# Performance work log

Hardware: AMD Instinct MI355X
Metric: run time of the kernel (lower is better)

Reference implementation:

```python
import jax, jax.numpy as jnp
import numpy as np

N, K, D_IN, D_H, D_A, N_CLS = 8192, 10, 1024, 512, 256, 4


def setup_inputs() -> dict:
    key = jax.random.key(0)
    ks = jax.random.split(key, 20)
    def lin(k, fan_in, shape):
        return jax.random.normal(k, shape, dtype=jnp.float32) / np.sqrt(fan_in)
    return {
        "x_path": jax.random.normal(ks[0], (N, D_IN), dtype=jnp.float32),
        "cluster_id": jax.random.randint(ks[1], (N,), 0, K),
        # per-cluster phi MLP (Linear 1024->512, ReLU, Linear 512->512, ReLU); dropout = eval identity
        "W1": lin(ks[2], D_IN, (K, D_IN, D_H)), "b1": jnp.zeros((K, D_H), jnp.float32),
        "W2": lin(ks[3], D_H, (K, D_H, D_H)), "b2": jnp.zeros((K, D_H), jnp.float32),
        # attention_net fc: Linear 512->512 + ReLU
        "fc_W": lin(ks[4], D_H, (D_H, D_H)), "fc_b": jnp.zeros((D_H,), jnp.float32),
        # Attn_Net_Gated: a=tanh(Va), b=sigmoid(Vb), A=(a*b)@Vc
        "Va": lin(ks[5], D_H, (D_H, D_A)), "ba": jnp.zeros((D_A,), jnp.float32),
        "Vb": lin(ks[6], D_H, (D_H, D_A)), "bb": jnp.zeros((D_A,), jnp.float32),
        "Vc": lin(ks[7], D_A, (D_A, 1)), "bc": jnp.zeros((1,), jnp.float32),
        # rho: Linear 512->256 + ReLU
        "rho_W": lin(ks[8], D_H, (D_H, D_A)), "rho_b": jnp.zeros((D_A,), jnp.float32),
        # classifier: Linear 256->4
        "cls_W": lin(ks[9], D_A, (D_A, N_CLS)), "cls_b": jnp.zeros((N_CLS,), jnp.float32),
    }


def reference(x_path, cluster_id, W1, b1, W2, b2, fc_W, fc_b,
              Va, ba, Vb, bb, Vc, bc, rho_W, rho_b, cls_W, cls_b):
    # mask[k, n] = 1 if patch n belongs to cluster k
    mask = (cluster_id[None, :] == jnp.arange(K)[:, None]).astype(x_path.dtype)  # [K, N]

    # per-cluster 2-layer MLP applied to all patches, masked mean-pool (= AdaptiveAvgPool1d(1))
    def phi(W1i, b1i, W2i, b2i):
        h = jax.nn.relu(x_path @ W1i + b1i)          # [N, 512]
        return jax.nn.relu(h @ W2i + b2i)            # [N, 512]
    y = jax.vmap(phi)(W1, b1, W2, b2)                # [K, N, 512]
    cnt = mask.sum(axis=1)                           # [K]
    pooled = jnp.einsum('kn,knd->kd', mask, y) / jnp.maximum(cnt, 1.0)[:, None]  # [K, 512]
    # empty cluster -> zeros (matches torch.zeros((1,512)) branch since b terms are zero via where)
    pooled = jnp.where(cnt[:, None] > 0, pooled, 0.0)

    # attention_net: fc + gated attention
    h = jax.nn.relu(pooled @ fc_W + fc_b)            # [K, 512]
    a = jnp.tanh(h @ Va + ba)                        # [K, 256]
    b = jax.nn.sigmoid(h @ Vb + bb)                  # [K, 256]
    A = (a * b) @ Vc + bc                            # [K, 1]
    A = jax.nn.softmax(A.T, axis=1)                  # [1, K]
    h_path = A @ h                                   # [1, 512]
    h_path = jax.nn.relu(h_path @ rho_W + rho_b)[0]  # [256]
    logits = (h_path @ cls_W + cls_b)[None, :]       # [1, 4]
    Y_hat = jnp.argmax(logits, axis=1, keepdims=True)
    hazards = jax.nn.sigmoid(logits)
    S = jnp.cumprod(1.0 - hazards, axis=1)
    return hazards, S, Y_hat
```

## Files before the change

kernel.cpp:

```cpp
#include <hip/hip_runtime.h>
#include <math.h>

#define NPATCH 8192
#define KC     10
#define DIN    1024
#define DH     512
#define DA     256
#define NCLS   4

#define TM  32

typedef unsigned short u16;
typedef short bf16x8 __attribute__((ext_vector_type(8)));
typedef float f32x4  __attribute__((ext_vector_type(4)));

#define OFF_CNT   0
#define OFF_BAR   48
#define OFF_IDX   64
#define OFF_PSUM  327744
#define OFF_H     348224
#define OFF_H2    368768
#define OFF_SRED  369792
#define OFF_W1P   373888
#define OFF_W2P   10859648

__device__ __forceinline__ u16 f2bf(float f) {
  union { float f; unsigned u; } v; v.f = f;
  unsigned r = (v.u + 0x7fffu + ((v.u >> 16) & 1u)) >> 16;
  return (u16)r;
}

__device__ __forceinline__ unsigned cvtpk(float lo, float hi) {
  unsigned r;
  asm("v_cvt_pk_bf16_f32 %0, %1, %2" : "=v"(r) : "v"(lo), "v"(hi));
  return r;
}

struct __align__(8) U16x4 { u16 x, y, z, w; };
union BF8U { bf16x8 v; unsigned u[4]; };

__device__ __forceinline__ void dma16(const u16* gp, u16* lp) {
  __builtin_amdgcn_global_load_lds(
      (const __attribute__((address_space(1))) void*)gp,
      (__attribute__((address_space(3))) void*)lp, 16, 0, 0);
}

#define W1_TILES (KC * (DIN / 32) * (DH / 32))
#define W2_TILES (KC * (DH / 32) * (DH / 32))
#define NB_BUCKET 32
#define WT_PER_BLK 4
#define NB_PREP (NB_BUCKET + (W1_TILES + W2_TILES) / WT_PER_BLK)

__global__ __launch_bounds__(256) void prep_kernel(
    const int* __restrict__ cid, int* __restrict__ cnt,
    int* __restrict__ idxlist, const float* __restrict__ W1,
    const float* __restrict__ W2, u16* __restrict__ W1p,
    u16* __restrict__ W2p, float* __restrict__ psum) {
  int b = blockIdx.x, t = threadIdx.x;
  if (b < NB_BUCKET) {
    int g = b * 256 + t;
    if (g < KC * DH) psum[g] = 0.f;
    __shared__ int lcnt[KC], lbase[KC];
    if (t < KC) lcnt[t] = 0;
    __syncthreads();
    int n = b * 256 + t;
    int k = cid[n];
    int myoff = atomicAdd(&lcnt[k], 1);
    __syncthreads();
    if (t < KC) lbase[t] = atomicAdd(&cnt[t], lcnt[t]);
    __syncthreads();
    idxlist[k * NPATCH + lbase[k] + myoff] = n;
  } else {
    __shared__ u16 tile[32][33];
#pragma unroll
    for (int it = 0; it < WT_PER_BLK; ++it) {
      int bb = (b - NB_BUCKET) * WT_PER_BLK + it;
      const float* src;
      u16* dst;
      if (bb < W1_TILES) {
        int k = bb / 512, rem = bb % 512;
        int kb = rem / 16, n0 = (rem % 16) * 32;
        src = W1 + (size_t)k * DIN * DH + (size_t)kb * 32 * DH + n0;
        dst = W1p + (((size_t)(k * 32 + kb) * 512 + n0) * 32);
      } else {
        int b2 = bb - W1_TILES;
        int k = b2 / 256, rem = b2 % 256;
        int kb = rem / 16, n0 = (rem % 16) * 32;
        src = W2 + (size_t)k * DH * DH + (size_t)kb * 32 * DH + n0;
        dst = W2p + (((size_t)(k * 16 + kb) * 512 + n0) * 32);
      }
      {
        int ki = t >> 3, n4 = (t & 7) * 4;
        float4 v = *(const float4*)&src[(size_t)ki * DH + n4];
        tile[ki][n4 + 0] = f2bf(v.x);
        tile[ki][n4 + 1] = f2bf(v.y);
        tile[ki][n4 + 2] = f2bf(v.z);
        tile[ki][n4 + 3] = f2bf(v.w);
      }
      __syncthreads();
      {
        int n = t >> 3, ki = (t & 7) * 4;
        U16x4 o = {tile[ki + 0][n], tile[ki + 1][n], tile[ki + 2][n],
                   tile[ki + 3][n]};
        *(U16x4*)&dst[(size_t)n * 32 + ki] = o;
      }
      __syncthreads();
    }
  }
}

__global__ __launch_bounds__(512) void phi_kernel(
    const float* __restrict__ x, const u16* __restrict__ W1p,
    const u16* __restrict__ W2p, const float* __restrict__ b1,
    const float* __restrict__ b2, const int* __restrict__ cnt,
    const int* __restrict__ idxlist, float* __restrict__ psum) {
  __shared__ __align__(16) u16 A0[TM * 512];
  __shared__ __align__(16) u16 A1[TM * 512];
  __shared__ __align__(16) u16 Bsh[2 * 8 * 4 * 512];

  const int tid = threadIdx.x;
  const int w = tid >> 6, lane = tid & 63;
  const int quad = lane >> 4, l16 = lane & 15;

  const int boff = (w * 64 + l16) * 32 + quad * 8;
  u16* myB0 = &Bsh[(size_t)w * 2048];
  u16* myB1 = &Bsh[16384 + (size_t)w * 2048];

  int cn[KC];
#pragma unroll
  for (int i = 0; i < KC; ++i) cn[i] = cnt[i];
  int G = 0;
#pragma unroll
  for (int i = 0; i < KC; ++i) G += (cn[i] + TM - 1) >> 5;

  const int s = blockIdx.x & 7, j = blockIdx.x >> 3;
  const int lo = (G * s) >> 3, hi = (G * (s + 1)) >> 3;

  for (int g = lo + j; g < hi; g += 64) {
    int kk = 0, rg = g, cntk = cn[0];
#pragma unroll
    for (int i = 0; i < KC - 1; ++i) {
      int nch = (cn[i] + TM - 1) >> 5;
      if (rg >= nch) { kk = i + 1; rg -= nch; cntk = cn[i + 1]; }
    }
    const int base = rg * TM;
    const int rot = (g * 5) & 31;
    const int rot2 = (g * 5) & 15;

    __syncthreads();

#pragma unroll
    for (int u8 = 0; u8 < 8; ++u8) {
      const int kh = u8 & 1;
      const int r = w * 4 + (u8 >> 1);
      BF8U o;
      if (base + r < cntk) {
        int src = idxlist[kk * NPATCH + base + r];
        const float4* xp =
            (const float4*)(x + (size_t)src * DIN + kh * 512 + lane * 8);
        float4 v0 = xp[0], v1 = xp[1];
        o.u[0] = cvtpk(v0.x, v0.y);
        o.u[1] = cvtpk(v0.z, v0.w);
        o.u[2] = cvtpk(v1.x, v1.y);
        o.u[3] = cvtpk(v1.z, v1.w);
      } else {
        o.u[0] = 0; o.u[1] = 0; o.u[2] = 0; o.u[3] = 0;
      }
      u16* dstbuf = kh ? A1 : A0;
      *(bf16x8*)&dstbuf[r * 512 + (lane ^ (r & 7)) * 8] = o.v;
    }
    __syncthreads();

    const u16* w1base = W1p + (size_t)(kk * 32) * 16384 + boff;
    const u16* w2base = W2p + (size_t)(kk * 16) * 16384 + boff;
#pragma unroll
    for (int p = 0; p < 2; ++p) {
      const u16* sb = w1base + (size_t)(((p + rot) & 31)) * 16384;
      u16* lb = p ? myB1 : myB0;
#pragma unroll
      for (int nt = 0; nt < 4; ++nt) dma16(sb + nt * 512, lb + nt * 512);
    }

    const f32x4 zero4 = {0.f, 0.f, 0.f, 0.f};
    f32x4 acc[2][4];
#pragma unroll
    for (int m = 0; m < 2; ++m)
#pragma unroll
      for (int nt = 0; nt < 4; ++nt) acc[m][nt] = zero4;

#pragma unroll
    for (int t = 0; t < 32; ++t) {
      asm volatile("s_waitcnt vmcnt(4)" ::: "memory");
      __builtin_amdgcn_sched_barrier(0);
      const u16* mb = (t & 1) ? myB1 : myB0;
      bf16x8 bf[4];
#pragma unroll
      for (int nt = 0; nt < 4; ++nt)
        bf[nt] = *(const bf16x8*)(mb + nt * 512 + lane * 8);
      const int ks = (t + rot) & 31;
      const u16* Ab = (ks < 16) ? A0 : A1;
      const int c8 = (((ks & 15) * 4 + quad) ^ (l16 & 7)) * 8;
      bf16x8 af0 = *(const bf16x8*)&Ab[l16 * 512 + c8];
      bf16x8 af1 = *(const bf16x8*)&Ab[(16 + l16) * 512 + c8];
      asm volatile("s_waitcnt lgkmcnt(0)" ::: "memory");
      __builtin_amdgcn_sched_barrier(0);
      {
        u16* lb = (t & 1) ? myB1 : myB0;
        const u16* sb = (t < 30)
            ? w1base + (size_t)(((t + 2 + rot) & 31)) * 16384
            : w2base + (size_t)(((t - 30 + rot2) & 15)) * 16384;
#pragma unroll
        for (int nt = 0; nt < 4; ++nt) dma16(sb + nt * 512, lb + nt * 512);
      }
#pragma unroll
      for (int nt = 0; nt < 4; ++nt) {
        acc[0][nt] = __builtin_amdgcn_mfma_f32_16x16x32_bf16(
            af0, bf[nt], acc[0][nt], 0, 0, 0);
        acc[1][nt] = __builtin_amdgcn_mfma_f32_16x16x32_bf16(
            af1, bf[nt], acc[1][nt], 0, 0, 0);
      }
    }
    __syncthreads();

#pragma unroll
    for (int m = 0; m < 2; ++m)
#pragma unroll
      for (int nt = 0; nt < 4; ++nt) {
        int c = w * 64 + nt * 16 + l16;
        float bias = b1[kk * DH + c];
#pragma unroll
        for (int r = 0; r < 4; ++r) {
          int row = m * 16 + quad * 4 + r;
          A0[row * 512 + (((c >> 3) ^ (row & 7)) * 8) + (c & 7)] =
              f2bf(fmaxf(acc[m][nt][r] + bias, 0.f));
        }
      }
    __syncthreads();

    f32x4 acc2[2][4];
#pragma unroll
    for (int m = 0; m < 2; ++m)
#pragma unroll
      for (int nt = 0; nt < 4; ++nt) acc2[m][nt] = zero4;

#pragma unroll
    for (int t = 0; t < 16; ++t) {
      if (t == 15) {
        asm volatile("s_waitcnt vmcnt(0)" ::: "memory");
      } else {
        asm volatile("s_waitcnt vmcnt(4)" ::: "memory");
      }
      __builtin_amdgcn_sched_barrier(0);
      const u16* mb = (t & 1) ? myB1 : myB0;
      bf16x8 bf[4];
#pragma unroll
      for (int nt = 0; nt < 4; ++nt)
        bf[nt] = *(const bf16x8*)(mb + nt * 512 + lane * 8);
      const int ks2 = (t + rot2) & 15;
      const int c8 = ((ks2 * 4 + quad) ^ (l16 & 7)) * 8;
      bf16x8 af0 = *(const bf16x8*)&A0[l16 * 512 + c8];
      bf16x8 af1 = *(const bf16x8*)&A0[(16 + l16) * 512 + c8];
      asm volatile("s_waitcnt lgkmcnt(0)" ::: "memory");
      __builtin_amdgcn_sched_barrier(0);
      if (t < 14) {
        u16* lb = (t & 1) ? myB1 : myB0;
        const u16* sb = w2base + (size_t)(((t + 2 + rot2) & 15)) * 16384;
#pragma unroll
        for (int nt = 0; nt < 4; ++nt) dma16(sb + nt * 512, lb + nt * 512);
      }
#pragma unroll
      for (int nt = 0; nt < 4; ++nt) {
        acc2[0][nt] = __builtin_amdgcn_mfma_f32_16x16x32_bf16(
            af0, bf[nt], acc2[0][nt], 0, 0, 0);
        acc2[1][nt] = __builtin_amdgcn_mfma_f32_16x16x32_bf16(
            af1, bf[nt], acc2[1][nt], 0, 0, 0);
      }
    }

    float vmask[2][4];
#pragma unroll
    for (int m = 0; m < 2; ++m)
#pragma unroll
      for (int r = 0; r < 4; ++r)
        vmask[m][r] = (base + m * 16 + quad * 4 + r < cntk) ? 1.f : 0.f;

#pragma unroll
    for (int nt = 0; nt < 4; ++nt) {
      int col = w * 64 + nt * 16 + l16;
      float bias = b2[kk * DH + col];
      float sv = 0.f;
#pragma unroll
      for (int m = 0; m < 2; ++m)
#pragma unroll
        for (int r = 0; r < 4; ++r)
          sv += vmask[m][r] * fmaxf(acc2[m][nt][r] + bias, 0.f);
      sv += __shfl_xor(sv, 16, 64);
      sv += __shfl_xor(sv, 32, 64);
      if (quad == 0) atomicAdd(&psum[kk * DH + col], sv);
    }
  }
}

#define NTB 64

__device__ __forceinline__ void bar_arrive_wait(int* bar) {
  __syncthreads();
  if (threadIdx.x == 0) {
    __threadfence();
    __hip_atomic_fetch_add(bar, 1, __ATOMIC_RELEASE, __HIP_MEMORY_SCOPE_AGENT);
    while (__hip_atomic_load(bar, __ATOMIC_ACQUIRE,
                             __HIP_MEMORY_SCOPE_AGENT) < NTB) {
      __builtin_amdgcn_s_sleep(1);
    }
  }
  __syncthreads();
}

__global__ __launch_bounds__(256) void tail_kernel(
    const float* __restrict__ psum, const int* __restrict__ cnt,
    const float* __restrict__ fcW, const float* __restrict__ fcb,
    const float* __restrict__ Va, const float* __restrict__ ba,
    const float* __restrict__ Vb, const float* __restrict__ bb_,
    const float* __restrict__ Vc, const float* __restrict__ rhoW,
    const float* __restrict__ rhob, const float* __restrict__ clsW,
    const float* __restrict__ clsb, float* __restrict__ hstore,
    float* __restrict__ sred, float* __restrict__ h2g,
    int* __restrict__ bar, float* __restrict__ out) {
  __shared__ float p_sh[KC * DH];
  __shared__ float r1[2560];
  __shared__ float r2[2560];
  __shared__ float invs[KC];
  __shared__ float gate_sh[4 * KC];
  __shared__ float ws_sh[KC];
  __shared__ float hp_sh[DH];
  const int tid = threadIdx.x;
  const int b = blockIdx.x;

  if (tid < KC) {
    int c = cnt[tid];
    invs[tid] = (c > 0) ? 1.f / (float)c : 0.f;
  }
  __syncthreads();
#pragma unroll
  for (int it = 0; it < KC * DH / 256; ++it) {
    int e = it * 256 + tid;
    p_sh[e] = psum[e] * invs[e >> 9];
  }
  __syncthreads();
  {
    const int jj = tid & 7, dq = tid >> 3;
    const int j0 = b * 8;
    float acc[KC];
#pragma unroll
    for (int k = 0; k < KC; ++k) acc[k] = 0.f;
#pragma unroll 4
    for (int i = 0; i < 16; ++i) {
      int d = dq * 16 + i;
      float wv = fcW[(size_t)d * DH + j0 + jj];
#pragma unroll
      for (int k = 0; k < KC; ++k) acc[k] = fmaf(p_sh[k * DH + d], wv, acc[k]);
    }
#pragma unroll
    for (int k = 0; k < KC; ++k) r1[(dq * 8 + jj) * KC + k] = acc[k];
    __syncthreads();
    if (tid < 8 * KC) {
      int jj2 = tid / KC, k = tid % KC;
      float s = 0.f;
#pragma unroll
      for (int q = 0; q < 32; ++q) s += r1[(q * 8 + jj2) * KC + k];
      hstore[k * DH + j0 + jj2] = fmaxf(s + fcb[j0 + jj2], 0.f);
    }
  }
  bar_arrive_wait(&bar[0]);

#pragma unroll
  for (int it = 0; it < KC * DH / 256; ++it) {
    int e = it * 256 + tid;
    p_sh[e] = hstore[e];
  }
  __syncthreads();
  {
    const int jj = tid & 3, dq = tid >> 2;
    const int j0 = b * 4;
    float sa[KC], sb[KC];
#pragma unroll
    for (int k = 0; k < KC; ++k) { sa[k] = 0.f; sb[k] = 0.f; }
#pragma unroll 4
    for (int i = 0; i < 8; ++i) {
      int d = dq * 8 + i;
      float va = Va[(size_t)d * DA + j0 + jj];
      float vb = Vb[(size_t)d * DA + j0 + jj];
#pragma unroll
      for (int k = 0; k < KC; ++k) {
        float h = p_sh[k * DH + d];
        sa[k] = fmaf(h, va, sa[k]);
        sb[k] = fmaf(h, vb, sb[k]);
      }
    }
#pragma unroll
    for (int k = 0; k < KC; ++k) {
      r1[(dq * 4 + jj) * KC + k] = sa[k];
      r2[(dq * 4 + jj) * KC + k] = sb[k];
    }
    __syncthreads();
    if (tid < 4 * KC) {
      int jj2 = tid / KC, k = tid % KC;
      float ta = 0.f, tb = 0.f;
#pragma unroll
      for (int q = 0; q < 64; ++q) {
        ta += r1[(q * 4 + jj2) * KC + k];
        tb += r2[(q * 4 + jj2) * KC + k];
      }
      float a = tanhf(ta + ba[j0 + jj2]);
      float g = 1.f / (1.f + expf(-(tb + bb_[j0 + jj2])));
      gate_sh[jj2 * KC + k] = a * g * Vc[j0 + jj2];
    }
    __syncthreads();
    if (tid < KC) {
      float s = 0.f;
#pragma unroll
      for (int jj2 = 0; jj2 < 4; ++jj2) s += gate_sh[jj2 * KC + tid];
      sred[b * 16 + tid] = s;
    }
  }
  bar_arrive_wait(&bar[1]);

  if (tid < KC) {
    float s = 0.f;
    for (int q = 0; q < NTB; ++q) s += sred[q * 16 + tid];
    ws_sh[tid] = s;
  }
  __syncthreads();
  if (tid == 0) {
    float m = -1e30f;
#pragma unroll
    for (int k2 = 0; k2 < KC; ++k2) m = fmaxf(m, ws_sh[k2]);
    float Z = 0.f;
#pragma unroll
    for (int k2 = 0; k2 < KC; ++k2) {
      float e = expf(ws_sh[k2] - m);
      ws_sh[k2] = e;
      Z += e;
    }
    float iZ = 1.f / Z;
#pragma unroll
    for (int k2 = 0; k2 < KC; ++k2) ws_sh[k2] *= iZ;
  }
  __syncthreads();
#pragma unroll
  for (int it = 0; it < 2; ++it) {
    int d = it * 256 + tid;
    float s = 0.f;
#pragma unroll
    for (int k2 = 0; k2 < KC; ++k2) s = fmaf(ws_sh[k2], p_sh[k2 * DH + d], s);
    hp_sh[d] = s;
  }
  __syncthreads();
  {
    const int jj = tid & 3, dq = tid >> 2;
    const int j0 = b * 4;
    float acc = 0.f;
#pragma unroll 4
    for (int i = 0; i < 8; ++i) {
      int d = dq * 8 + i;
      acc = fmaf(hp_sh[d], rhoW[(size_t)d * DA + j0 + jj], acc);
    }
    r1[dq * 4 + jj] = acc;
    __syncthreads();
    if (tid < 4) {
      float s = 0.f;
#pragma unroll
      for (int q = 0; q < 64; ++q) s += r1[q * 4 + tid];
      h2g[j0 + tid] = fmaxf(s + rhob[j0 + tid], 0.f);
    }
  }

  if (b != 0) {
    __syncthreads();
    if (tid == 0) {
      __threadfence();
      __hip_atomic_fetch_add(&bar[2], 1, __ATOMIC_RELEASE,
                             __HIP_MEMORY_SCOPE_AGENT);
    }
    return;
  }
  bar_arrive_wait(&bar[2]);
  {
    float h = h2g[tid];
#pragma unroll
    for (int c = 0; c < NCLS; ++c)
      r1[c * 256 + tid] = h * clsW[(size_t)tid * NCLS + c];
    __syncthreads();
    for (int s = 128; s > 0; s >>= 1) {
      if (tid < s) {
#pragma unroll
        for (int c = 0; c < NCLS; ++c)
          r1[c * 256 + tid] += r1[c * 256 + tid + s];
      }
      __syncthreads();
    }
    if (tid == 0) {
      float lg[NCLS], hz[NCLS];
      int best = 0;
#pragma unroll
      for (int c = 0; c < NCLS; ++c) {
        lg[c] = r1[c * 256] + clsb[c];
        hz[c] = 1.f / (1.f + expf(-lg[c]));
        if (lg[c] > lg[best]) best = c;
      }
      float S = 1.f;
#pragma unroll
      for (int c = 0; c < NCLS; ++c) out[c] = hz[c];
#pragma unroll
      for (int c = 0; c < NCLS; ++c) {
        S *= (1.f - hz[c]);
        out[NCLS + c] = S;
      }
      out[2 * NCLS] = (float)best;
    }
  }
}

extern "C" void kernel_launch(void* const* d_in, const int* in_sizes, int n_in,
                              void* d_out, int out_size, void* d_ws,
                              size_t ws_size, hipStream_t stream) {
  const float* x    = (const float*)d_in[0];
  const int*   cid  = (const int*)d_in[1];
  const float* W1   = (const float*)d_in[2];
  const float* b1   = (const float*)d_in[3];
  const float* W2   = (const float*)d_in[4];
  const float* b2   = (const float*)d_in[5];
  const float* fcW  = (const float*)d_in[6];
  const float* fcb  = (const float*)d_in[7];
  const float* Va   = (const float*)d_in[8];
  const float* ba   = (const float*)d_in[9];
  const float* Vb   = (const float*)d_in[10];
  const float* bb_  = (const float*)d_in[11];
  const float* Vc   = (const float*)d_in[12];
  const float* rhoW = (const float*)d_in[14];
  const float* rhob = (const float*)d_in[15];
  const float* clsW = (const float*)d_in[16];
  const float* clsb = (const float*)d_in[17];
  float* out = (float*)d_out;

  char* ws = (char*)d_ws;
  int*   cnt     = (int*)(ws + OFF_CNT);
  int*   bar     = (int*)(ws + OFF_BAR);
  int*   idxlist = (int*)(ws + OFF_IDX);
  float* psum    = (float*)(ws + OFF_PSUM);
  float* hstore  = (float*)(ws + OFF_H);
  float* h2g     = (float*)(ws + OFF_H2);
  float* sred    = (float*)(ws + OFF_SRED);
  u16*   W1p     = (u16*)(ws + OFF_W1P);
  u16*   W2p     = (u16*)(ws + OFF_W2P);

  (void)hipMemsetAsync(cnt, 0, 64, stream);
  prep_kernel<<<NB_PREP, 256, 0, stream>>>(cid, cnt, idxlist, W1, W2, W1p, W2p,
                                           psum);
  phi_kernel<<<512, 512, 0, stream>>>(x, W1p, W2p, b1, b2, cnt, idxlist, psum);
  tail_kernel<<<NTB, 256, 0, stream>>>(psum, cnt, fcW, fcb, Va, ba, Vb, bb_,
                                       Vc, rhoW, rhob, clsW, clsb, hstore,
                                       sred, h2g, bar, out);
}
```

Measured before the change: 211.4 us.

## Split fused phi MLP into pack, layer-1 and layer-2 GEMM kernels with 128x128 tiles

Measured after the change: 211.5 us. No clear change (+0.0%).

```diff
diff --git a/kernel.cpp b/kernel.cpp
--- a/kernel.cpp
+++ b/kernel.cpp
@@ -7,8 +7,6 @@
 #define DH     512
 #define DA     256
 #define NCLS   4
-
-#define TM  32
 
 typedef unsigned short u16;
 typedef short bf16x8 __attribute__((ext_vector_type(8)));
@@ -23,6 +21,8 @@
 #define OFF_SRED  369792
 #define OFF_W1P   373888
 #define OFF_W2P   10859648
+#define OFF_XC    16102528
+#define OFF_H1    32879744
 
 __device__ __forceinline__ u16 f2bf(float f) {
   union { float f; unsigned u; } v; v.f = f;
@@ -30,14 +30,7 @@
   return (u16)r;
 }
 
-__device__ __forceinline__ unsigned cvtpk(float lo, float hi) {
-  unsigned r;
-  asm("v_cvt_pk_bf16_f32 %0, %1, %2" : "=v"(r) : "v"(lo), "v"(hi));
-  return r;
-}
-
 struct __align__(8) U16x4 { u16 x, y, z, w; };
-union BF8U { bf16x8 v; unsigned u[4]; };
 
 __device__ __forceinline__ void dma16(const u16* gp, u16* lp) {
   __builtin_amdgcn_global_load_lds(
@@ -102,202 +95,268 @@
         int n = t >> 3, ki = (t & 7) * 4;
         U16x4 o = {tile[ki + 0][n], tile[ki + 1][n], tile[ki + 2][n],
                    tile[ki + 3][n]};
-        *(U16x4*)&dst[(size_t)n * 32 + ki] = o;
+        int kis = ki ^ (((n >> 1) & 3) << 3);
+        *(U16x4*)&dst[(size_t)n * 32 + kis] = o;
       }
       __syncthreads();
     }
   }
 }
 
-__global__ __launch_bounds__(512) void phi_kernel(
-    const float* __restrict__ x, const u16* __restrict__ W1p,
-    const u16* __restrict__ W2p, const float* __restrict__ b1,
-    const float* __restrict__ b2, const int* __restrict__ cnt,
-    const int* __restrict__ idxlist, float* __restrict__ psum) {
-  __shared__ __align__(16) u16 A0[TM * 512];
-  __shared__ __align__(16) u16 A1[TM * 512];
-  __shared__ __align__(16) u16 Bsh[2 * 8 * 4 * 512];
+__global__ __launch_bounds__(256) void pack_kernel(
+    const float* __restrict__ x, const int* __restrict__ cnt,
+    const int* __restrict__ idxlist, u16* __restrict__ xc) {
+  const int b = blockIdx.x, t = threadIdx.x;
+  int cb[KC];
+  {
+    int a = 0;
+#pragma unroll
+    for (int i = 0; i < KC; ++i) { cb[i] = a; a += cnt[i]; }
+  }
+  int row = b * 32 + (t >> 3);
+  int k = 0;
+#pragma unroll
+  for (int i = 1; i < KC; ++i) k = (row >= cb[i]) ? i : k;
+  int src = idxlist[k * NPATCH + (row - cb[k])];
+  const float4* xp = (const float4*)(x + (size_t)src * DIN + (t & 7) * 128);
+  U16x4* dst = (U16x4*)(xc + (size_t)row * DIN + (t & 7) * 128);
+#pragma unroll
+  for (int j = 0; j < 32; ++j) {
+    float4 v = xp[j];
+    U16x4 o = {f2bf(v.x), f2bf(v.y), f2bf(v.z), f2bf(v.w)};
+    dst[j] = o;
+  }
+}
+
+
+__global__ __launch_bounds__(256, 2) void phi1_kernel(
+    const u16* __restrict__ xc, const u16* __restrict__ W1p,
+    const float* __restrict__ b1, const int* __restrict__ cnt,
+    u16* __restrict__ h1) {
+  const int slice = blockIdx.x, k = blockIdx.y, chunk = blockIdx.z;
+  const int cntk = cnt[k];
+  const int row0 = chunk * 128;
+  if (row0 >= cntk) return;
+  int cbase = 0;
+#pragma unroll
+  for (int i = 0; i < KC - 1; ++i) cbase += (i < k) ? cnt[i] : 0;
 
   const int tid = threadIdx.x;
   const int w = tid >> 6, lane = tid & 63;
   const int quad = lane >> 4, l16 = lane & 15;
-
-  const int boff = (w * 64 + l16) * 32 + quad * 8;
-  u16* myB0 = &Bsh[(size_t)w * 2048];
-  u16* myB1 = &Bsh[16384 + (size_t)w * 2048];
-
-  int cn[KC];
-#pragma unroll
-  for (int i = 0; i < KC; ++i) cn[i] = cnt[i];
-  int G = 0;
-#pragma unroll
-  for (int i = 0; i < KC; ++i) G += (cn[i] + TM - 1) >> 5;
-
-  const int s = blockIdx.x & 7, j = blockIdx.x >> 3;
-  const int lo = (G * s) >> 3, hi = (G * (s + 1)) >> 3;
-
-  for (int g = lo + j; g < hi; g += 64) {
-    int kk = 0, rg = g, cntk = cn[0];
-#pragma unroll
-    for (int i = 0; i < KC - 1; ++i) {
-      int nch = (cn[i] + TM - 1) >> 5;
-      if (rg >= nch) { kk = i + 1; rg -= nch; cntk = cn[i + 1]; }
-    }
-    const int base = rg * TM;
-    const int rot = (g * 5) & 31;
-    const int rot2 = (g * 5) & 15;
-
-    __syncthreads();
-
-#pragma unroll
-    for (int u8 = 0; u8 < 8; ++u8) {
-      const int kh = u8 & 1;
-      const int r = w * 4 + (u8 >> 1);
-      BF8U o;
-      if (base + r < cntk) {
-        int src = idxlist[kk * NPATCH + base + r];
-        const float4* xp =
-            (const float4*)(x + (size_t)src * DIN + kh * 512 + lane * 8);
-        float4 v0 = xp[0], v1 = xp[1];
-        o.u[0] = cvtpk(v0.x, v0.y);
-        o.u[1] = cvtpk(v0.z, v0.w);
-        o.u[2] = cvtpk(v1.x, v1.y);
-        o.u[3] = cvtpk(v1.z, v1.w);
-      } else {
-        o.u[0] = 0; o.u[1] = 0; o.u[2] = 0; o.u[3] = 0;
-      }
-      u16* dstbuf = kh ? A1 : A0;
-      *(bf16x8*)&dstbuf[r * 512 + (lane ^ (r & 7)) * 8] = o.v;
-    }
-    __syncthreads();
-
-    const u16* w1base = W1p + (size_t)(kk * 32) * 16384 + boff;
-    const u16* w2base = W2p + (size_t)(kk * 16) * 16384 + boff;
-#pragma unroll
-    for (int p = 0; p < 2; ++p) {
-      const u16* sb = w1base + (size_t)(((p + rot) & 31)) * 16384;
-      u16* lb = p ? myB1 : myB0;
-#pragma unroll
-      for (int nt = 0; nt < 4; ++nt) dma16(sb + nt * 512, lb + nt * 512);
-    }
-
-    const f32x4 zero4 = {0.f, 0.f, 0.f, 0.f};
-    f32x4 acc[2][4];
-#pragma unroll
-    for (int m = 0; m < 2; ++m)
-#pragma unroll
-      for (int nt = 0; nt < 4; ++nt) acc[m][nt] = zero4;
-
-#pragma unroll
-    for (int t = 0; t < 32; ++t) {
+  const int wr = w >> 1, wc = w & 1;
+  const int rl = lane >> 2, gl = lane & 3;
+
+  __shared__ __align__(16) u16 lds[17408];
+  u16* As = lds;
+  u16* Bs = lds + 8192;
+
+  const size_t arow0 = (size_t)(cbase + row0);
+
+#pragma unroll
+  for (int jj = 0; jj < 2; ++jj) {
+    int rg = w * 2 + jj;
+    int row_l = rg * 16 + rl;
+    size_t grow = arow0 + row_l; if (grow > 8191) grow = 8191;
+    int g = gl ^ ((row_l >> 1) & 3);
+    dma16(xc + grow * DIN + g * 8, As + rg * 512);
+  }
+#pragma unroll
+  for (int jj = 0; jj < 2; ++jj) {
+    int cg = w * 2 + jj;
+    int col_l = cg * 16 + rl;
+    dma16(W1p + ((size_t)(k * 32) * 512 + slice * 128 + col_l) * 32 + gl * 8,
+          Bs + cg * 512);
+  }
+
+  const f32x4 zero4 = {0.f, 0.f, 0.f, 0.f};
+  f32x4 acc[4][4];
+#pragma unroll
+  for (int fr = 0; fr < 4; ++fr)
+#pragma unroll
+    for (int fc = 0; fc < 4; ++fc) acc[fr][fc] = zero4;
+
+  for (int t = 0; t < 32; ++t) {
+    const int buf = t & 1;
+    if (t < 31) {
+      const int tn = t + 1, bn = buf ^ 1;
+#pragma unroll
+      for (int jj = 0; jj < 2; ++jj) {
+        int rg = w * 2 + jj;
+        int row_l = rg * 16 + rl;
+        size_t grow = arow0 + row_l; if (grow > 8191) grow = 8191;
+        int g = gl ^ ((row_l >> 1) & 3);
+        dma16(xc + grow * DIN + tn * 32 + g * 8, As + bn * 4096 + rg * 512);
+      }
+#pragma unroll
+      for (int jj = 0; jj < 2; ++jj) {
+        int cg = w * 2 + jj;
+        int col_l = cg * 16 + rl;
+        dma16(W1p + ((size_t)(k * 32 + tn) * 512 + slice * 128 + col_l) * 32 +
+                  gl * 8,
+              Bs + bn * 4096 + cg * 512);
+      }
       asm volatile("s_waitcnt vmcnt(4)" ::: "memory");
-      __builtin_amdgcn_sched_barrier(0);
-      const u16* mb = (t & 1) ? myB1 : myB0;
-      bf16x8 bf[4];
-#pragma unroll
-      for (int nt = 0; nt < 4; ++nt)
-        bf[nt] = *(const bf16x8*)(mb + nt * 512 + lane * 8);
-      const int ks = (t + rot) & 31;
-      const u16* Ab = (ks < 16) ? A0 : A1;
-      const int c8 = (((ks & 15) * 4 + quad) ^ (l16 & 7)) * 8;
-      bf16x8 af0 = *(const bf16x8*)&Ab[l16 * 512 + c8];
-      bf16x8 af1 = *(const bf16x8*)&Ab[(16 + l16) * 512 + c8];
-      asm volatile("s_waitcnt lgkmcnt(0)" ::: "memory");
-      __builtin_amdgcn_sched_barrier(0);
-      {
-        u16* lb = (t & 1) ? myB1 : myB0;
-        const u16* sb = (t < 30)
-            ? w1base + (size_t)(((t + 2 + rot) & 31)) * 16384
-            : w2base + (size_t)(((t - 30 + rot2) & 15)) * 16384;
-#pragma unroll
-        for (int nt = 0; nt < 4; ++nt) dma16(sb + nt * 512, lb + nt * 512);
-      }
-#pragma unroll
-      for (int nt = 0; nt < 4; ++nt) {
-        acc[0][nt] = __builtin_amdgcn_mfma_f32_16x16x32_bf16(
-            af0, bf[nt], acc[0][nt], 0, 0, 0);
-        acc[1][nt] = __builtin_amdgcn_mfma_f32_16x16x32_bf16(
-            af1, bf[nt], acc[1][nt], 0, 0, 0);
-      }
-    }
-    __syncthreads();
-
-#pragma unroll
-    for (int m = 0; m < 2; ++m)
-#pragma unroll
-      for (int nt = 0; nt < 4; ++nt) {
-        int c = w * 64 + nt * 16 + l16;
-        float bias = b1[kk * DH + c];
-#pragma unroll
-        for (int r = 0; r < 4; ++r) {
-          int row = m * 16 + quad * 4 + r;
-          A0[row * 512 + (((c >> 3) ^ (row & 7)) * 8) + (c & 7)] =
-              f2bf(fmaxf(acc[m][nt][r] + bias, 0.f));
-        }
-      }
-    __syncthreads();
-
-    f32x4 acc2[2][4];
-#pragma unroll
-    for (int m = 0; m < 2; ++m)
-#pragma unroll
-      for (int nt = 0; nt < 4; ++nt) acc2[m][nt] = zero4;
-
-#pragma unroll
-    for (int t = 0; t < 16; ++t) {
-      if (t == 15) {
-        asm volatile("s_waitcnt vmcnt(0)" ::: "memory");
-      } else {
-        asm volatile("s_waitcnt vmcnt(4)" ::: "memory");
-      }
-      __builtin_amdgcn_sched_barrier(0);
-      const u16* mb = (t & 1) ? myB1 : myB0;
-      bf16x8 bf[4];
-#pragma unroll
-      for (int nt = 0; nt < 4; ++nt)
-        bf[nt] = *(const bf16x8*)(mb + nt * 512 + lane * 8);
-      const int ks2 = (t + rot2) & 15;
-      const int c8 = ((ks2 * 4 + quad) ^ (l16 & 7)) * 8;
-      bf16x8 af0 = *(const bf16x8*)&A0[l16 * 512 + c8];
-      bf16x8 af1 = *(const bf16x8*)&A0[(16 + l16) * 512 + c8];
-      asm volatile("s_waitcnt lgkmcnt(0)" ::: "memory");
-      __builtin_amdgcn_sched_barrier(0);
-      if (t < 14) {
-        u16* lb = (t & 1) ? myB1 : myB0;
-        const u16* sb = w2base + (size_t)(((t + 2 + rot2) & 15)) * 16384;
-#pragma unroll
-        for (int nt = 0; nt < 4; ++nt) dma16(sb + nt * 512, lb + nt * 512);
-      }
-#pragma unroll
-      for (int nt = 0; nt < 4; ++nt) {
-        acc2[0][nt] = __builtin_amdgcn_mfma_f32_16x16x32_bf16(
-            af0, bf[nt], acc2[0][nt], 0, 0, 0);
-        acc2[1][nt] = __builtin_amdgcn_mfma_f32_16x16x32_bf16(
-            af1, bf[nt], acc2[1][nt], 0, 0, 0);
-      }
-    }
-
-    float vmask[2][4];
-#pragma unroll
-    for (int m = 0; m < 2; ++m)
-#pragma unroll
-      for (int r = 0; r < 4; ++r)
-        vmask[m][r] = (base + m * 16 + quad * 4 + r < cntk) ? 1.f : 0.f;
-
-#pragma unroll
-    for (int nt = 0; nt < 4; ++nt) {
-      int col = w * 64 + nt * 16 + l16;
-      float bias = b2[kk * DH + col];
-      float sv = 0.f;
-#pragma unroll
-      for (int m = 0; m < 2; ++m)
-#pragma unroll
-        for (int r = 0; r < 4; ++r)
-          sv += vmask[m][r] * fmaxf(acc2[m][nt][r] + bias, 0.f);
-      sv += __shfl_xor(sv, 16, 64);
-      sv += __shfl_xor(sv, 32, 64);
-      if (quad == 0) atomicAdd(&psum[kk * DH + col], sv);
-    }
+    } else {
+      asm volatile("s_waitcnt vmcnt(0)" ::: "memory");
+    }
+    __syncthreads();
+    bf16x8 af[4], bfr[4];
+#pragma unroll
+    for (int fr = 0; fr < 4; ++fr) {
+      int row = wr * 64 + fr * 16 + l16;
+      af[fr] = *(const bf16x8*)&As[buf * 4096 + row * 32 +
+                                   ((quad ^ ((row >> 1) & 3)) << 3)];
+    }
+#pragma unroll
+    for (int fc = 0; fc < 4; ++fc) {
+      int col = wc * 64 + fc * 16 + l16;
+      bfr[fc] = *(const bf16x8*)&Bs[buf * 4096 + col * 32 +
+                                    ((quad ^ ((col >> 1) & 3)) << 3)];
+    }
+#pragma unroll
+    for (int fr = 0; fr < 4; ++fr)
+#pragma unroll
+      for (int fc = 0; fc < 4; ++fc)
+        acc[fr][fc] = __builtin_amdgcn_mfma_f32_16x16x32_bf16(
+            af[fr], bfr[fc], acc[fr][fc], 0, 0, 0);
+    __syncthreads();
+  }
+
+#pragma unroll
+  for (int fr = 0; fr < 4; ++fr)
+#pragma unroll
+    for (int fc = 0; fc < 4; ++fc) {
+      int col = wc * 64 + fc * 16 + l16;
+      float bias = b1[k * DH + slice * 128 + col];
+#pragma unroll
+      for (int r = 0; r < 4; ++r) {
+        int row = wr * 64 + fr * 16 + quad * 4 + r;
+        lds[row * 136 + col] = f2bf(fmaxf(acc[fr][fc][r] + bias, 0.f));
+      }
+    }
+  __syncthreads();
+  {
+    int row = tid >> 1, half = tid & 1;
+    if (row0 + row < cntk) {
+      u16* dst = h1 + (arow0 + row) * DH + slice * 128 + half * 64;
+      const u16* srcl = &lds[row * 136 + half * 64];
+#pragma unroll
+      for (int j = 0; j < 8; ++j)
+        *(bf16x8*)(dst + j * 8) = *(const bf16x8*)(srcl + j * 8);
+    }
+  }
+}
+
+__global__ __launch_bounds__(256, 2) void phi2_kernel(
+    const u16* __restrict__ h1, const u16* __restrict__ W2p,
+    const float* __restrict__ b2, const int* __restrict__ cnt,
+    float* __restrict__ psum) {
+  const int slice = blockIdx.x, k = blockIdx.y, chunk = blockIdx.z;
+  const int cntk = cnt[k];
+  const int row0 = chunk * 128;
+  if (row0 >= cntk) return;
+  int cbase = 0;
+#pragma unroll
+  for (int i = 0; i < KC - 1; ++i) cbase += (i < k) ? cnt[i] : 0;
+
+  const int tid = threadIdx.x;
+  const int w = tid >> 6, lane = tid & 63;
+  const int quad = lane >> 4, l16 = lane & 15;
+  const int wr = w >> 1, wc = w & 1;
+  const int rl = lane >> 2, gl = lane & 3;
+
+  __shared__ __align__(16) u16 lds[16384];
+  u16* As = lds;
+  u16* Bs = lds + 8192;
+
+  const size_t arow0 = (size_t)(cbase + row0);
+
+#pragma unroll
+  for (int jj = 0; jj < 2; ++jj) {
+    int rg = w * 2 + jj;
+    int row_l = rg * 16 + rl;
+    size_t grow = arow0 + row_l; if (grow > 8191) grow = 8191;
+    int g = gl ^ ((row_l >> 1) & 3);
+    dma16(h1 + grow * DH + g * 8, As + rg * 512);
+  }
+#pragma unroll
+  for (int jj = 0; jj < 2; ++jj) {
+    int cg = w * 2 + jj;
+    int col_l = cg * 16 + rl;
+    dma16(W2p + ((size_t)(k * 16) * 512 + slice * 128 + col_l) * 32 + gl * 8,
+          Bs + cg * 512);
+  }
+
+  const f32x4 zero4 = {0.f, 0.f, 0.f, 0.f};
+  f32x4 acc[4][4];
+#pragma unroll
+  for (int fr = 0; fr < 4; ++fr)
+#pragma unroll
+    for (int fc = 0; fc < 4; ++fc) acc[fr][fc] = zero4;
+
+  for (int t = 0; t < 16; ++t) {
+    const int buf = t & 1;
+    if (t < 15) {
+      const int tn = t + 1, bn = buf ^ 1;
+#pragma unroll
+      for (int jj = 0; jj < 2; ++jj) {
+        int rg = w * 2 + jj;
+        int row_l = rg * 16 + rl;
+        size_t grow = arow0 + row_l; if (grow > 8191) grow = 8191;
+        int g = gl ^ ((row_l >> 1) & 3);
+        dma16(h1 + grow * DH + tn * 32 + g * 8, As + bn * 4096 + rg * 512);
+      }
+#pragma unroll
+      for (int jj = 0; jj < 2; ++jj) {
+        int cg = w * 2 + jj;
+        int col_l = cg * 16 + rl;
+        dma16(W2p + ((size_t)(k * 16 + tn) * 512 + slice * 128 + col_l) * 32 +
+                  gl * 8,
+              Bs + bn * 4096 + cg * 512);
+      }
+      asm volatile("s_waitcnt vmcnt(4)" ::: "memory");
+    } else {
+      asm volatile("s_waitcnt vmcnt(0)" ::: "memory");
+    }
+    __syncthreads();
+    bf16x8 af[4], bfr[4];
+#pragma unroll
+    for (int fr = 0; fr < 4; ++fr) {
+      int row = wr * 64 + fr * 16 + l16;
+      af[fr] = *(const bf16x8*)&As[buf * 4096 + row * 32 +
+                                   ((quad ^ ((row >> 1) & 3)) << 3)];
+    }
+#pragma unroll
+    for (int fc = 0; fc < 4; ++fc) {
+      int col = wc * 64 + fc * 16 + l16;
+      bfr[fc] = *(const bf16x8*)&Bs[buf * 4096 + col * 32 +
+                                    ((quad ^ ((col >> 1) & 3)) << 3)];
+    }
+#pragma unroll
+    for (int fr = 0; fr < 4; ++fr)
+#pragma unroll
+      for (int fc = 0; fc < 4; ++fc)
+        acc[fr][fc] = __builtin_amdgcn_mfma_f32_16x16x32_bf16(
+            af[fr], bfr[fc], acc[fr][fc], 0, 0, 0);
+    __syncthreads();
+  }
+
+#pragma unroll
+  for (int fc = 0; fc < 4; ++fc) {
+    int col = wc * 64 + fc * 16 + l16;
+    float bias = b2[k * DH + slice * 128 + col];
+    float sv = 0.f;
+#pragma unroll
+    for (int fr = 0; fr < 4; ++fr)
+#pragma unroll
+      for (int r = 0; r < 4; ++r) {
+        int row = row0 + wr * 64 + fr * 16 + quad * 4 + r;
+        sv += (row < cntk) ? fmaxf(acc[fr][fc][r] + bias, 0.f) : 0.f;
+      }
+    sv += __shfl_xor(sv, 16, 64);
+    sv += __shfl_xor(sv, 32, 64);
+    if (quad == 0) atomicAdd(&psum[k * DH + slice * 128 + col], sv);
   }
 }
 
@@ -553,11 +612,15 @@
   float* sred    = (float*)(ws + OFF_SRED);
   u16*   W1p     = (u16*)(ws + OFF_W1P);
   u16*   W2p     = (u16*)(ws + OFF_W2P);
+  u16*   xc      = (u16*)(ws + OFF_XC);
+  u16*   h1      = (u16*)(ws + OFF_H1);
 
   (void)hipMemsetAsync(cnt, 0, 64, stream);
   prep_kernel<<<NB_PREP, 256, 0, stream>>>(cid, cnt, idxlist, W1, W2, W1p, W2p,
                                            psum);
-  phi_kernel<<<512, 512, 0, stream>>>(x, W1p, W2p, b1, b2, cnt, idxlist, psum);
+  pack_kernel<<<NPATCH / 32, 256, 0, stream>>>(x, cnt, idxlist, xc);
+  phi1_kernel<<<dim3(4, KC, 64), 256, 0, stream>>>(xc, W1p, b1, cnt, h1);
+  phi2_kernel<<<dim3(4, KC, 64), 256, 0, stream>>>(h1, W2p, b2, cnt, psum);
   tail_kernel<<<NTB, 256, 0, stream>>>(psum, cnt, fcW, fcb, Va, ba, Vb, bb_,
                                        Vc, rhoW, rhob, clsW, clsb, hstore,
                                        sred, h2g, bar, out);
```
